# Kernel optimization log

Hardware: AMD Instinct MI355X
Metric: run time of the kernel (lower is better)

## Reference

```python
import jax, jax.numpy as jnp
import numpy as np
from jax import lax

STATE_SIZE = 80
HIDDEN = 512
NC = 1
H = W = 32
STEPS = 64  # steps_range=(64,64)
THRESH = 0.01


def _maxpool3(x):
    # MaxPool2d(3, stride=1, padding=1) on NCHW
    return lax.reduce_window(x, -jnp.inf, lax.max, (1, 1, 3, 3), (1, 1, 1, 1), 'SAME')


def _conv3x3(x, w, b):
    y = lax.conv_general_dilated(x, w, (1, 1), 'SAME',
                                 dimension_numbers=('NCHW', 'OIHW', 'NCHW'))
    return y + b[None, :, None, None]


def _conv1x1(x, w, b):
    # w: (O, I, 1, 1) -> pointwise einsum
    return jnp.einsum('oi,bihw->bohw', w[:, :, 0, 0], x) + b[None, :, None, None]


def setup_inputs() -> dict:
    key = jax.random.key(0)
    ks = jax.random.split(key, 7)
    z = jax.random.normal(ks[0], (8, 100, 1, 1), dtype=jnp.float32)
    W1 = jax.random.normal(ks[1], (HIDDEN, STATE_SIZE, 3, 3), jnp.float32) / np.sqrt(STATE_SIZE * 9)
    b1 = jax.random.normal(ks[2], (HIDDEN,), jnp.float32) * 0.01
    W2 = jax.random.normal(ks[3], (HIDDEN, HIDDEN, 1, 1), jnp.float32) / np.sqrt(HIDDEN)
    b2 = jax.random.normal(ks[4], (HIDDEN,), jnp.float32) * 0.01
    # original code zero-inits the last conv; use small random weights so grads flow
    W3 = jax.random.normal(ks[5], (STATE_SIZE, HIDDEN, 1, 1), jnp.float32) * (0.01 / np.sqrt(HIDDEN))
    b3 = jax.random.normal(ks[6], (STATE_SIZE,), jnp.float32) * 0.001
    return {'z': z, 'W1': W1, 'b1': b1, 'W2': W2, 'b2': b2, 'W3': W3, 'b3': b3}


def _forward(z, W1, b1, W2, b2, W3, b3):
    N = z.shape[0]
    cH, cW = H // 2, W // 2
    state = jnp.zeros((N, STATE_SIZE, H, W), dtype=z.dtype)
    init_hidden = z[:, :STATE_SIZE - 1, 0, 0]  # (N, 79)
    state = state.at[:, 1:, cH, cW].set(init_hidden)
    state = state.at[:, 0, cH, cW].set(1.0)

    keys = jax.random.split(jax.random.key(42), STEPS)

    def ca_step(state, step_key):
        pre_living = _maxpool3(state[:, 0:1]) > THRESH
        perception = _conv3x3(state, W1, b1)
        h = jax.nn.relu(_conv1x1(perception, W2, b2))
        updates = _conv1x1(h, W3, b3)
        # stochastic update with p=1 (rand < 1 is always True, kept for fidelity)
        mask = jax.random.uniform(step_key, (state.shape[0], 1, H, W)) < 1.0
        state = state + mask.astype(state.dtype) * updates
        post_living = _maxpool3(state[:, 0:1]) > THRESH
        living = (post_living & pre_living).astype(state.dtype)
        return state * living, None

    state, _ = lax.scan(ca_step, state, keys)
    return state[:, :NC]  # (N, 1, H, W)


def reference(z, W1, b1, W2, b2, W3, b3):
    return _forward(z, W1, b1, W2, b2, W3, b3)
```

## Files before the change

kernel.cpp:

```cpp
#include <hip/hip_runtime.h>


#define NPIX 8192
#define T_ALIVE 0.01f

typedef _Float16 f16;
typedef __attribute__((ext_vector_type(8)))  _Float16 h8_t;
typedef __attribute__((ext_vector_type(4)))  _Float16 h4_t;
typedef __attribute__((ext_vector_type(16))) float    fx16;

__global__ __launch_bounds__(256) void tr512(
    const float* __restrict__ W2, float* __restrict__ W2T)
{
    __shared__ float t[32][33];
    const int bx = blockIdx.x & 15, by = blockIdx.x >> 4;
    const int x = threadIdx.x & 31, y8 = threadIdx.x >> 5;
#pragma unroll
    for (int r = 0; r < 32; r += 8)
        t[r + y8][x] = W2[(size_t)(by * 32 + r + y8) * 512 + bx * 32 + x];
    __syncthreads();
#pragma unroll
    for (int r = 0; r < 32; r += 8)
        W2T[(size_t)(bx * 32 + r + y8) * 512 + by * 32 + x] = t[x][r + y8];
}

__global__ __launch_bounds__(256) void wc32(
    const float* __restrict__ W2T, const float* __restrict__ W1,
    float* __restrict__ Wc)
{
    __shared__ float As[16][32];
    __shared__ float Bs[16][32];
    const int tid = threadIdx.x;
    const int ty = tid >> 3, tx = tid & 7;
    const int m0 = blockIdx.y * 32, n0 = blockIdx.x * 32;
    float acc[4] = {0.f, 0.f, 0.f, 0.f};

    for (int k0 = 0; k0 < 512; k0 += 16) {
#pragma unroll
        for (int t = 0; t < 2; ++t) {
            const int idx = tid + t * 256;
            const int r = idx >> 5, c = idx & 31;
            As[r][c] = W2T[(size_t)(k0 + r) * 512 + m0 + c];
            const int n = n0 + c;
            Bs[r][c] = (n < 720) ? W1[(size_t)(k0 + r) * 720 + n] : 0.f;
        }
        __syncthreads();
#pragma unroll
        for (int kk = 0; kk < 16; ++kk) {
            const float a = As[kk][ty];
#pragma unroll
            for (int j = 0; j < 4; ++j)
                acc[j] = fmaf(a, Bs[kk][tx * 4 + j], acc[j]);
        }
        __syncthreads();
    }
    const int m = m0 + ty;
#pragma unroll
    for (int j = 0; j < 4; ++j) {
        const int n = n0 + tx * 4 + j;
        if (n < 720) Wc[(size_t)m * 720 + n] = acc[j];
    }
}

__global__ __launch_bounds__(256) void bc_k(
    const float* __restrict__ W2, const float* __restrict__ b1,
    const float* __restrict__ b2, float* __restrict__ bc)
{
    const int m = blockIdx.x * 256 + threadIdx.x;
    if (m >= 512) return;
    float a = b2[m];
    for (int h = 0; h < 512; ++h) a += W2[m * 512 + h] * b1[h];
    bc[m] = a;
}

__global__ __launch_bounds__(256) void swz_wc2(
    const float* __restrict__ Wc, f16* __restrict__ Wcsw2)
{
    const int idx = blockIdx.x * 256 + threadIdx.x;
    if (idx >= 45 * 16 * 64) return;
    const int lane = idx & 63;
    const int t = idx >> 6;
    const int mtg = t & 15, ks = t >> 4;
    const int m = mtg * 32 + (lane & 31);
    const int k0 = ks * 16 + (lane >> 5) * 8;
    h8_t v;
#pragma unroll
    for (int j = 0; j < 8; ++j) {
        const int kp = k0 + j;
        const int tap = kp / 80, ci = kp - tap * 80;
        v[j] = (f16)Wc[(size_t)m * 720 + ci * 9 + tap];
    }
    *(h8_t*)(Wcsw2 + (size_t)idx * 8) = v;
}

__global__ __launch_bounds__(256) void swz_w32(
    const float* __restrict__ W3, f16* __restrict__ W3sw2)
{
    const int idx = blockIdx.x * 256 + threadIdx.x;
    if (idx >= 32 * 3 * 64) return;
    const int lane = idx & 63;
    const int t = idx >> 6;
    const int mt = t % 3, ks2 = t / 3;
    const int m = mt * 32 + (lane & 31);
    const int k0 = ks2 * 16 + (lane >> 5) * 8;
    h8_t v;
#pragma unroll
    for (int j = 0; j < 8; ++j)
        v[j] = (f16)((m < 80) ? W3[(size_t)m * 512 + k0 + j] : 0.f);
    *(h8_t*)(W3sw2 + (size_t)idx * 8) = v;
}

__global__ __launch_bounds__(256) void seed_k(
    const float* __restrict__ z, float* __restrict__ Sf32,
    f16* __restrict__ Smf16)
{
    const int idx = blockIdx.x * 256 + threadIdx.x;
    if (idx >= 640) return;
    const int b = idx / 80, c = idx - b * 80;
    const int n = b * 1024 + 16 * 32 + 16;
    const float v = (c == 0) ? 1.f : z[b * 100 + (c - 1)];
    Sf32[(size_t)c * NPIX + n] = v;
    Smf16[(size_t)n * 80 + c] = (f16)v;
}

__global__ __launch_bounds__(512) void kA(
    const f16* __restrict__ Smf16, const f16* __restrict__ Wcsw2,
    const float* __restrict__ bc, const f16* __restrict__ W3sw2,
    const float* __restrict__ b3,
    const float* __restrict__ Sold, float* __restrict__ U)
{
    __shared__ f16   msT[8160];
    __shared__ f16   Hsw[16384];
    __shared__ float bcL[512];
    __shared__ float b3L[80];

    const int tid = threadIdx.x;
    const int lane = tid & 63, w = tid >> 6;
    const int li = lane & 31, q2 = lane >> 5;
    const int blk = blockIdx.x;
    const int b = blk >> 5, y = blk & 31;
    const int gb = b * 1024;

    if (tid < 512) bcL[tid] = bc[tid];
    if (tid < 80)  b3L[tid] = b3[tid];

    for (int idx = tid; idx < 1020; idx += 512) {
        const int p = idx / 10, cc = idx - p * 10;
        const int r = p / 34, xi = p - r * 34;
        const int gx = xi - 1, yy = y - 1 + r;
        h8_t v;
        if (((unsigned)yy < 32u) & ((unsigned)gx < 32u)) {
            v = *(const h8_t*)(Smf16 + (size_t)(gb + yy * 32 + gx) * 80 + cc * 8);
        } else {
#pragma unroll
            for (int j = 0; j < 8; ++j) v[j] = (f16)0.f;
        }
        *(h8_t*)(msT + (size_t)(cc * 102 + p) * 8) = v;
    }
    __syncthreads();

    int pxh[9];
#pragma unroll
    for (int t = 0; t < 9; ++t)
        pxh[t] = ((t / 3) * 34 + li + (t % 3)) * 8;

    fx16 acc[2];
#pragma unroll
    for (int i = 0; i < 2; ++i)
#pragma unroll
        for (int r = 0; r < 16; ++r) acc[i][r] = 0.f;

    h8_t abuf[8][2];
#pragma unroll
    for (int pk = 0; pk < 8; ++pk)
#pragma unroll
        for (int i = 0; i < 2; ++i)
            abuf[pk][i] = *(const h8_t*)(Wcsw2 +
                (((size_t)pk * 16 + (w * 2 + i)) * 64 + lane) * 8);

#pragma unroll
    for (int ks = 0; ks < 45; ++ks) {
        const int o0 = 2 * ks, o1 = 2 * ks + 1;
        const int a0 = (o0 % 10) * 816 + pxh[o0 / 10];
        const int a1 = (o1 % 10) * 816 + pxh[o1 / 10];
        const h8_t bf = *(const h8_t*)(msT + (q2 ? a1 : a0));
        h8_t av[2];
#pragma unroll
        for (int i = 0; i < 2; ++i) av[i] = abuf[ks & 7][i];
        if (ks + 8 < 45) {
#pragma unroll
            for (int i = 0; i < 2; ++i)
                abuf[ks & 7][i] = *(const h8_t*)(Wcsw2 +
                    (((size_t)(ks + 8) * 16 + (w * 2 + i)) * 64 + lane) * 8);
        }
#pragma unroll
        for (int i = 0; i < 2; ++i)
            acc[i] = __builtin_amdgcn_mfma_f32_32x32x16_f16(
                av[i], bf, acc[i], 0, 0, 0);
    }

#pragma unroll
    for (int i = 0; i < 2; ++i) {
#pragma unroll
        for (int aa = 0; aa < 4; ++aa) {
            const int chl = i * 32 + 8 * aa + 4 * q2;
            const int co = w * 8 + i * 4 + aa;
            h4_t v4;
#pragma unroll
            for (int rb = 0; rb < 4; ++rb)
                v4[rb] = (f16)fmaxf(acc[i][aa * 4 + rb] + bcL[w * 64 + chl + rb], 0.f);
            *(h4_t*)(Hsw + ((size_t)co * 32 + li) * 8 + 4 * q2) = v4;
        }
    }
    __syncthreads();

    if (w < 3) {
        const int mt = w;
        h8_t ar[8];
#pragma unroll
        for (int pk = 0; pk < 8; ++pk)
            ar[pk] = *(const h8_t*)(W3sw2 +
                (((size_t)pk * 3 + mt) * 64 + lane) * 8);

        fx16 acc3;
#pragma unroll
        for (int r = 0; r < 16; ++r) acc3[r] = 0.f;
#pragma unroll
        for (int ks2 = 0; ks2 < 32; ++ks2) {
            const h8_t bf = *(const h8_t*)(Hsw +
                ((size_t)(ks2 * 2 + q2) * 32 + li) * 8);
            const h8_t a = ar[ks2 & 7];
            if (ks2 + 8 < 32)
                ar[ks2 & 7] = *(const h8_t*)(W3sw2 +
                    (((size_t)(ks2 + 8) * 3 + mt) * 64 + lane) * 8);
            acc3 = __builtin_amdgcn_mfma_f32_32x32x16_f16(a, bf, acc3, 0, 0, 0);
        }

        const size_t px = (size_t)(gb + y * 32 + li);
#pragma unroll
        for (int aa = 0; aa < 4; ++aa)
#pragma unroll
            for (int rb = 0; rb < 4; ++rb) {
                const int ch = mt * 32 + rb + 8 * aa + 4 * q2;
                if (ch < 80) {
                    const size_t idx = (size_t)ch * NPIX + px;
                    U[idx] = Sold[idx] + acc3[aa * 4 + rb] + b3L[ch];
                }
            }
    }
}

__global__ __launch_bounds__(256) void kB(
    const float* __restrict__ U, const float* __restrict__ Sold,
    float* __restrict__ Snew, f16* __restrict__ Smf16,
    float* __restrict__ dout, int last)
{
    __shared__ float alphaO3[96];
    __shared__ float alphaN3[96];
    __shared__ float livef[32];

    const int tid = threadIdx.x;
    const int blk = blockIdx.x;
    const int b = blk >> 5, y = blk & 31;
    const int gb = b * 1024;
    const int base = gb + y * 32;

    if (tid < 96) {
        const int r = tid >> 5, x = tid & 31, yy = y - 1 + r;
        if ((unsigned)yy < 32u) {
            alphaO3[tid] = Sold[gb + yy * 32 + x];
            alphaN3[tid] = U[gb + yy * 32 + x];
        } else {
            alphaO3[tid] = -1e30f;
            alphaN3[tid] = -1e30f;
        }
    }
    __syncthreads();

    if (tid < 32) {
        float mN = -1e30f, mO = -1e30f;
#pragma unroll
        for (int r = 0; r < 3; ++r)
#pragma unroll
            for (int dx = -1; dx <= 1; ++dx) {
                const int xx = tid + dx;
                if ((unsigned)xx < 32u) {
                    mN = fmaxf(mN, alphaN3[r * 32 + xx]);
                    mO = fmaxf(mO, alphaO3[r * 32 + xx]);
                }
            }
        livef[tid] = (mN > T_ALIVE && mO > T_ALIVE) ? 1.f : 0.f;
    }
    __syncthreads();

    for (int q = tid; q < 640; q += 256) {
        const int cq = q >> 5, x = q & 31;
        const float lv = livef[x];
        const size_t pxg = (size_t)(base + x);
        h4_t v4;
        float v0 = 0.f;
#pragma unroll
        for (int rb = 0; rb < 4; ++rb) {
            const int ch = cq * 4 + rb;
            const size_t idx = (size_t)ch * NPIX + pxg;
            const float v = U[idx] * lv;
            Snew[idx] = v;
            v4[rb] = (f16)v;
            if (rb == 0) v0 = v;
        }
        *(h4_t*)(Smf16 + pxg * 80 + cq * 4) = v4;
        if (last && cq == 0) dout[pxg] = v0;
    }
}

extern "C" void kernel_launch(void* const* d_in, const int* in_sizes, int n_in,
                              void* d_out, int out_size, void* d_ws, size_t ws_size,
                              hipStream_t stream)
{
    const float* z  = (const float*)d_in[0];
    const float* W1 = (const float*)d_in[1];
    const float* b1 = (const float*)d_in[2];
    const float* W2 = (const float*)d_in[3];
    const float* b2 = (const float*)d_in[4];
    const float* W3 = (const float*)d_in[5];
    const float* b3 = (const float*)d_in[6];

    char* ws = (char*)d_ws;
    float* S0    = (float*)ws;  ws += (size_t)80 * NPIX * 4;
    float* S1    = (float*)ws;  ws += (size_t)80 * NPIX * 4;
    f16*   Sm0   = (f16*)ws;   ws += (size_t)NPIX * 80 * 2;
    f16*   Sm1   = (f16*)ws;   ws += (size_t)NPIX * 80 * 2;
    float* Ubuf  = (float*)ws;  ws += (size_t)80 * NPIX * 4;
    float* bc    = (float*)ws;  ws += 512 * 4;
    float* Wc    = (float*)ws;  ws += (size_t)512 * 720 * 4;
    float* W2T   = (float*)ws;  ws += (size_t)512 * 512 * 4;
    f16*   Wcsw2 = (f16*)ws;   ws += (size_t)45 * 16 * 64 * 8 * 2;
    f16*   W3sw2 = (f16*)ws;   ws += (size_t)32 * 3 * 64 * 8 * 2;

    hipMemsetAsync(S0, 0, (size_t)80 * NPIX * 4, stream);
    hipMemsetAsync(Sm0, 0, (size_t)NPIX * 80 * 2, stream);
    seed_k<<<3, 256, 0, stream>>>(z, S0, Sm0);
    tr512<<<256, 256, 0, stream>>>(W2, W2T);
    wc32<<<dim3(23, 16), 256, 0, stream>>>(W2T, W1, Wc);
    bc_k<<<2, 256, 0, stream>>>(W2, b1, b2, bc);
    swz_wc2<<<180, 256, 0, stream>>>(Wc, Wcsw2);
    swz_w32<<<24, 256, 0, stream>>>(W3, W3sw2);

    float* Scur = S0;  float* Snxt = S1;
    f16*   Mcur = Sm0; f16*   Mnxt = Sm1;
    for (int s = 0; s < 64; ++s) {
        kA<<<256, 512, 0, stream>>>(Mcur, Wcsw2, bc, W3sw2, b3, Scur, Ubuf);
        kB<<<256, 256, 0, stream>>>(Ubuf, Scur, Snxt, Mnxt,
                                    (float*)d_out, (s == 63) ? 1 : 0);
        float* t = Scur; Scur = Snxt; Snxt = t;
        f16*   m = Mcur; Mcur = Mnxt; Mnxt = m;
    }
}
```

Measured before the change: 1.147 ms.

## Fuse living-mask apply into next step's conv kernel, drop separate kB pass

Removes the per-step kB kernel. Each kA now recomputes the previous step's living mask from a 5-row halo of the unmasked update and the previous masked alpha channel, applies it while building the fp16 shared tile, and writes the masked alpha for the next step. A small final kernel applies the last mask to produce the output. This halves the launches per step and removes the extra fp32 and fp16 state round trips. In exchange, kA reads fp32 channel-planar data and converts it to fp16 with scattered shared-memory stores, and the halo mask work is duplicated across blocks.

```diff
diff --git a/kernel.cpp b/kernel.cpp
--- a/kernel.cpp
+++ b/kernel.cpp
@@ -111,28 +111,28 @@
 }
 
 __global__ __launch_bounds__(256) void seed_k(
-    const float* __restrict__ z, float* __restrict__ Sf32,
-    f16* __restrict__ Smf16)
+    const float* __restrict__ z, float* __restrict__ U0)
 {
     const int idx = blockIdx.x * 256 + threadIdx.x;
     if (idx >= 640) return;
     const int b = idx / 80, c = idx - b * 80;
     const int n = b * 1024 + 16 * 32 + 16;
-    const float v = (c == 0) ? 1.f : z[b * 100 + (c - 1)];
-    Sf32[(size_t)c * NPIX + n] = v;
-    Smf16[(size_t)n * 80 + c] = (f16)v;
+    U0[(size_t)c * NPIX + n] = (c == 0) ? 1.f : z[b * 100 + (c - 1)];
 }
 
 __global__ __launch_bounds__(512) void kA(
-    const f16* __restrict__ Smf16, const f16* __restrict__ Wcsw2,
-    const float* __restrict__ bc, const f16* __restrict__ W3sw2,
-    const float* __restrict__ b3,
-    const float* __restrict__ Sold, float* __restrict__ U)
+    const float* __restrict__ Uprev, const float* __restrict__ MaPrev,
+    const f16* __restrict__ Wcsw2, const float* __restrict__ bc,
+    const f16* __restrict__ W3sw2, const float* __restrict__ b3,
+    float* __restrict__ Ucur, float* __restrict__ MaCur, int first)
 {
     __shared__ f16   msT[8160];
     __shared__ f16   Hsw[16384];
     __shared__ float bcL[512];
     __shared__ float b3L[80];
+    __shared__ float aN5[160];
+    __shared__ float aO5[160];
+    __shared__ float live3[96];
 
     const int tid = threadIdx.x;
     const int lane = tid & 63, w = tid >> 6;
@@ -141,21 +141,57 @@
     const int b = blk >> 5, y = blk & 31;
     const int gb = b * 1024;
 
-    if (tid < 512) bcL[tid] = bc[tid];
-    if (tid < 80)  b3L[tid] = b3[tid];
-
-    for (int idx = tid; idx < 1020; idx += 512) {
-        const int p = idx / 10, cc = idx - p * 10;
-        const int r = p / 34, xi = p - r * 34;
-        const int gx = xi - 1, yy = y - 1 + r;
-        h8_t v;
-        if (((unsigned)yy < 32u) & ((unsigned)gx < 32u)) {
-            v = *(const h8_t*)(Smf16 + (size_t)(gb + yy * 32 + gx) * 80 + cc * 8);
-        } else {
-#pragma unroll
-            for (int j = 0; j < 8; ++j) v[j] = (f16)0.f;
-        }
-        *(h8_t*)(msT + (size_t)(cc * 102 + p) * 8) = v;
+    bcL[tid] = bc[tid];
+    if (tid < 80) b3L[tid] = b3[tid];
+    if (tid < 160) {
+        const int r5 = tid >> 5, x = tid & 31, yy = y - 2 + r5;
+        const bool inb = (unsigned)yy < 32u;
+        aN5[tid] = inb ? Uprev[gb + yy * 32 + x]  : -1e30f;
+        aO5[tid] = inb ? MaPrev[gb + yy * 32 + x] : -1e30f;
+    }
+    __syncthreads();
+
+    if (tid < 96) {
+        const int r3 = tid >> 5, x = tid & 31;
+        const int yy = y - 1 + r3;
+        float lv = 0.f;
+        if ((unsigned)yy < 32u) {
+            if (first) lv = 1.f;
+            else {
+                float mN = -1e30f, mO = -1e30f;
+#pragma unroll
+                for (int dy = 0; dy <= 2; ++dy)
+#pragma unroll
+                    for (int dx = -1; dx <= 1; ++dx) {
+                        const int xx = x + dx;
+                        if ((unsigned)xx < 32u) {
+                            mN = fmaxf(mN, aN5[(r3 + dy) * 32 + xx]);
+                            mO = fmaxf(mO, aO5[(r3 + dy) * 32 + xx]);
+                        }
+                    }
+                lv = (mN > T_ALIVE && mO > T_ALIVE) ? 1.f : 0.f;
+            }
+        }
+        live3[tid] = lv;
+    }
+    __syncthreads();
+
+    if (tid < 32)
+        MaCur[gb + y * 32 + tid] = Uprev[gb + y * 32 + tid] * live3[32 + tid];
+
+    if (tid < 480) {
+        const int c = tid / 6, rem = tid - c * 6;
+        const int r = rem >> 1, p = r * 34 + ((rem & 1) ? 33 : 0);
+        msT[(size_t)(((c >> 3) * 102 + p) * 8) + (c & 7)] = (f16)0.f;
+    }
+    for (int idx = tid; idx < 7680; idx += 512) {
+        const int c = idx / 96, rem = idx - c * 96;
+        const int r = rem >> 5, x = rem & 31;
+        const int yy = y - 1 + r;
+        float v = 0.f;
+        if ((unsigned)yy < 32u)
+            v = Uprev[(size_t)c * NPIX + gb + yy * 32 + x] * live3[r * 32 + x];
+        msT[(size_t)(((c >> 3) * 102 + r * 34 + x + 1) * 8) + (c & 7)] = (f16)v;
     }
     __syncthreads();
 
@@ -237,6 +273,7 @@
         }
 
         const size_t px = (size_t)(gb + y * 32 + li);
+        const float lv = live3[32 + li];
 #pragma unroll
         for (int aa = 0; aa < 4; ++aa)
 #pragma unroll
@@ -244,73 +281,35 @@
                 const int ch = mt * 32 + rb + 8 * aa + 4 * q2;
                 if (ch < 80) {
                     const size_t idx = (size_t)ch * NPIX + px;
-                    U[idx] = Sold[idx] + acc3[aa * 4 + rb] + b3L[ch];
+                    Ucur[idx] = Uprev[idx] * lv + acc3[aa * 4 + rb] + b3L[ch];
                 }
             }
     }
 }
 
-__global__ __launch_bounds__(256) void kB(
-    const float* __restrict__ U, const float* __restrict__ Sold,
-    float* __restrict__ Snew, f16* __restrict__ Smf16,
-    float* __restrict__ dout, int last)
-{
-    __shared__ float alphaO3[96];
-    __shared__ float alphaN3[96];
-    __shared__ float livef[32];
-
-    const int tid = threadIdx.x;
-    const int blk = blockIdx.x;
-    const int b = blk >> 5, y = blk & 31;
+__global__ __launch_bounds__(256) void fin_k(
+    const float* __restrict__ U, const float* __restrict__ Ma,
+    float* __restrict__ dout)
+{
+    const int n = blockIdx.x * 256 + threadIdx.x;
+    const int b = n >> 10, r = n & 1023;
+    const int y = r >> 5, x = r & 31;
     const int gb = b * 1024;
-    const int base = gb + y * 32;
-
-    if (tid < 96) {
-        const int r = tid >> 5, x = tid & 31, yy = y - 1 + r;
-        if ((unsigned)yy < 32u) {
-            alphaO3[tid] = Sold[gb + yy * 32 + x];
-            alphaN3[tid] = U[gb + yy * 32 + x];
-        } else {
-            alphaO3[tid] = -1e30f;
-            alphaN3[tid] = -1e30f;
-        }
-    }
-    __syncthreads();
-
-    if (tid < 32) {
-        float mN = -1e30f, mO = -1e30f;
-#pragma unroll
-        for (int r = 0; r < 3; ++r)
-#pragma unroll
-            for (int dx = -1; dx <= 1; ++dx) {
-                const int xx = tid + dx;
-                if ((unsigned)xx < 32u) {
-                    mN = fmaxf(mN, alphaN3[r * 32 + xx]);
-                    mO = fmaxf(mO, alphaO3[r * 32 + xx]);
-                }
-            }
-        livef[tid] = (mN > T_ALIVE && mO > T_ALIVE) ? 1.f : 0.f;
-    }
-    __syncthreads();
-
-    for (int q = tid; q < 640; q += 256) {
-        const int cq = q >> 5, x = q & 31;
-        const float lv = livef[x];
-        const size_t pxg = (size_t)(base + x);
-        h4_t v4;
-        float v0 = 0.f;
-#pragma unroll
-        for (int rb = 0; rb < 4; ++rb) {
-            const int ch = cq * 4 + rb;
-            const size_t idx = (size_t)ch * NPIX + pxg;
-            const float v = U[idx] * lv;
-            Snew[idx] = v;
-            v4[rb] = (f16)v;
-            if (rb == 0) v0 = v;
-        }
-        *(h4_t*)(Smf16 + pxg * 80 + cq * 4) = v4;
-        if (last && cq == 0) dout[pxg] = v0;
-    }
+    float mN = -1e30f, mO = -1e30f;
+#pragma unroll
+    for (int dy = -1; dy <= 1; ++dy) {
+        const int yy = y + dy;
+        if ((unsigned)yy >= 32u) continue;
+#pragma unroll
+        for (int dx = -1; dx <= 1; ++dx) {
+            const int xx = x + dx;
+            if ((unsigned)xx >= 32u) continue;
+            mN = fmaxf(mN, U[gb + yy * 32 + xx]);
+            mO = fmaxf(mO, Ma[gb + yy * 32 + xx]);
+        }
+    }
+    const float lv = (mN > T_ALIVE && mO > T_ALIVE) ? 1.f : 0.f;
+    dout[n] = U[n] * lv;
 }
 
 extern "C" void kernel_launch(void* const* d_in, const int* in_sizes, int n_in,
@@ -326,33 +325,31 @@
     const float* b3 = (const float*)d_in[6];
 
     char* ws = (char*)d_ws;
-    float* S0    = (float*)ws;  ws += (size_t)80 * NPIX * 4;
-    float* S1    = (float*)ws;  ws += (size_t)80 * NPIX * 4;
-    f16*   Sm0   = (f16*)ws;   ws += (size_t)NPIX * 80 * 2;
-    f16*   Sm1   = (f16*)ws;   ws += (size_t)NPIX * 80 * 2;
-    float* Ubuf  = (float*)ws;  ws += (size_t)80 * NPIX * 4;
+    float* U0    = (float*)ws;  ws += (size_t)80 * NPIX * 4;
+    float* U1    = (float*)ws;  ws += (size_t)80 * NPIX * 4;
+    float* Ma0   = (float*)ws;  ws += NPIX * 4;
+    float* Ma1   = (float*)ws;  ws += NPIX * 4;
     float* bc    = (float*)ws;  ws += 512 * 4;
     float* Wc    = (float*)ws;  ws += (size_t)512 * 720 * 4;
     float* W2T   = (float*)ws;  ws += (size_t)512 * 512 * 4;
     f16*   Wcsw2 = (f16*)ws;   ws += (size_t)45 * 16 * 64 * 8 * 2;
     f16*   W3sw2 = (f16*)ws;   ws += (size_t)32 * 3 * 64 * 8 * 2;
 
-    hipMemsetAsync(S0, 0, (size_t)80 * NPIX * 4, stream);
-    hipMemsetAsync(Sm0, 0, (size_t)NPIX * 80 * 2, stream);
-    seed_k<<<3, 256, 0, stream>>>(z, S0, Sm0);
+    hipMemsetAsync(U0, 0, (size_t)80 * NPIX * 4, stream);
+    seed_k<<<3, 256, 0, stream>>>(z, U0);
     tr512<<<256, 256, 0, stream>>>(W2, W2T);
     wc32<<<dim3(23, 16), 256, 0, stream>>>(W2T, W1, Wc);
     bc_k<<<2, 256, 0, stream>>>(W2, b1, b2, bc);
     swz_wc2<<<180, 256, 0, stream>>>(Wc, Wcsw2);
     swz_w32<<<24, 256, 0, stream>>>(W3, W3sw2);
 
-    float* Scur = S0;  float* Snxt = S1;
-    f16*   Mcur = Sm0; f16*   Mnxt = Sm1;
-    for (int s = 0; s < 64; ++s) {
-        kA<<<256, 512, 0, stream>>>(Mcur, Wcsw2, bc, W3sw2, b3, Scur, Ubuf);
-        kB<<<256, 256, 0, stream>>>(Ubuf, Scur, Snxt, Mnxt,
-                                    (float*)d_out, (s == 63) ? 1 : 0);
-        float* t = Scur; Scur = Snxt; Snxt = t;
-        f16*   m = Mcur; Mcur = Mnxt; Mnxt = m;
-    }
-}
+    float* Ub[2]  = {U0, U1};
+    float* Mab[2] = {Ma0, Ma1};
+    for (int i = 0; i < 64; ++i) {
+        kA<<<256, 512, 0, stream>>>(Ub[i & 1], Mab[(i + 1) & 1],
+                                    Wcsw2, bc, W3sw2, b3,
+                                    Ub[(i + 1) & 1], Mab[i & 1],
+                                    (i == 0) ? 1 : 0);
+    }
+    fin_k<<<32, 256, 0, stream>>>(Ub[0], Mab[1], (float*)d_out);
+}
```

Result: slower. 1.331 ms (+16.0%).
